# Performance work log

Measured on AMD Instinct MI355X. Metric: run time of the kernel, lower is better.

The kernel has to match this reference:

```python
import jax, jax.numpy as jnp
import numpy as np

# Reconstructed Int8Conv2d semantics (repo internals not shown):
#  - input quantized to int8 with running scale: q = clip(round(x/scale), -128, 127)
#  - int8 weights (integer-valued fp32 here), int32 accumulation via conv
#  - dequantize with scale*W_SCALE; propagated scale gains a fixed requant
#    factor RQ so next layer's int8 quantization stays in range.
W_SCALE = 0.05   # per-layer weight quantization scale
RQ = 16.0        # fixed requantization gain folded into propagated scale
INIT_SCALE = 0.05


def _round(x):
    return jnp.round(x)


def quant8(x, scale):
    return jnp.clip(_round(x / scale), -128.0, 127.0)


def conv2d(x, w, stride):
    # x: NHWC, w: HWIO, VALID padding
    return jax.lax.conv_general_dilated(
        x, w, window_strides=(stride, stride), padding='VALID',
        dimension_numbers=('NHWC', 'HWIO', 'NHWC'))


def int8_conv(scale, x, w8, stride=1):
    x8 = quant8(x, scale)                 # emulated int8
    acc = conv2d(x8, w8, stride)          # emulated int32 accumulate
    y = acc * (scale * W_SCALE)           # dequantize
    return scale * W_SCALE * RQ, y


def qmax_pool2d(x, k, s):
    return jax.lax.reduce_window(
        x, -jnp.inf, jax.lax.max,
        window_dimensions=(1, k, k, 1), window_strides=(1, s, s, 1),
        padding='VALID')


def setup_inputs() -> dict:
    key = jax.random.key(0)
    ks = jax.random.split(key, 5)
    B = 32768
    x = jax.random.uniform(ks[0], (B, 784), dtype=jnp.float32)
    # int8-valued weights stored as float32 (small range keeps int8 path unsaturated)
    w1 = jax.random.randint(ks[1], (3, 3, 4, 4), -8, 9).astype(jnp.float32)
    w2 = jax.random.randint(ks[2], (3, 3, 4, 4), -8, 9).astype(jnp.float32)
    w3 = jax.random.randint(ks[3], (3, 3, 4, 4), -8, 9).astype(jnp.float32)
    w4 = jax.random.randint(ks[4], (1, 1, 4, 12), -8, 9).astype(jnp.float32)
    return {'x': x, 'w1': w1, 'w2': w2, 'w3': w3, 'w4': w4}


def reference(x, w1, w2, w3, w4):
    B = x.shape[0]
    # reshape(-1,1,28,28,1) + pad last dim to 4  ==  NHWC with C=4 (3 zero channels)
    h = x.reshape(B, 28, 28, 1)
    h = jnp.pad(h, ((0, 0), (0, 0), (0, 0), (0, 3)))

    scale, h = int8_conv(INIT_SCALE, h, w1)      # -> 26x26x4
    h = qmax_pool2d(h, 2, 2)                      # -> 13x13
    h = jax.nn.relu(h)
    scale, h = int8_conv(scale, h, w2)            # -> 11x11
    h = qmax_pool2d(h, 2, 2)                      # -> 5x5
    h = jax.nn.relu(h)
    scale, h = int8_conv(scale, h, w3)            # -> 3x3
    h = qmax_pool2d(h, 3, 1)                      # -> 1x1
    h = jax.nn.relu(h)
    scale, h = int8_conv(scale, h, w4)            # -> 1x1x12
    h = jax.nn.relu(h)
    # (B,1,1,12) -> (B,12) -> drop last 2 -> (B,10)
    return h.reshape(B, 12)[:, :10]
```

## Files before the change

### kernel.cpp

```cpp
#include <hip/hip_runtime.h>
#include <hip/hip_bf16.h>

#define IPB 4

constexpr double dDQ1 = 0.05 * 0.05;
constexpr double dDQ2 = 0.05 * 0.05 * 16.0 * 0.05;
constexpr double dDQ3 = 0.05 * 0.05 * 16.0 * 0.05 * 16.0 * 0.05;
constexpr double dDQ4 = 0.05 * 0.05 * 16.0 * 0.05 * 16.0 * 0.05 * 16.0 * 0.05;

#define R1f 20.0f
#define R2f 25.0f
#define R3f 31.2499980926513671875f
#define R4f 39.0625f

#if __has_builtin(__builtin_amdgcn_sdot4)
__device__ __forceinline__ int dot4(int a, int b, int c) {
    return __builtin_amdgcn_sdot4(a, b, c, false);
}
#else
__device__ __forceinline__ int dot4(int a, int b, int c) {
    #pragma unroll
    for (int k = 0; k < 4; ++k)
        c += (int)(signed char)(a >> (8 * k)) * (int)(signed char)(b >> (8 * k));
    return c;
}
#endif

__device__ __forceinline__ void wave_fence() {
    __builtin_amdgcn_fence(__ATOMIC_ACQ_REL, "workgroup");
}

__device__ __forceinline__ float bfr(float f) {
    unsigned int u = __builtin_bit_cast(unsigned int, f);
    u += 0x7fffu + ((u >> 16) & 1u);
    u &= 0xffff0000u;
    return __builtin_bit_cast(float, u);
}

__device__ __forceinline__ int packq(float4 v) {
    int b0 = (int)rintf(v.x * R1f);
    int b1 = (int)rintf(v.y * R1f);
    int b2 = (int)rintf(v.z * R1f);
    int b3 = (int)rintf(v.w * R1f);
    return b0 | (b1 << 8) | (b2 << 16) | (b3 << 24);
}

__global__ void qcnn_prep(const float* __restrict__ w1, const float* __restrict__ w2,
                          const float* __restrict__ w3, const float* __restrict__ w4,
                          int* __restrict__ wpk) {
    int t = threadIdx.x;
    if (t < 24) {
        int oc = t / 6, rem = t % 6, r = rem >> 1, sh = rem & 1;
        int v = 0;
        #pragma unroll
        for (int k = 0; k < 4; ++k) {
            int kw = k - sh;
            int w = (kw >= 0 && kw < 3) ? (int)w1[(r * 3 + kw) * 16 + oc] : 0;
            v |= (w & 0xff) << (8 * k);
        }
        wpk[t] = v;
    } else if (t < 60) {
        int e = t - 24, tap = e >> 2, oc = e & 3, v = 0;
        #pragma unroll
        for (int k = 0; k < 4; ++k) v |= (((int)w2[tap * 16 + k * 4 + oc]) & 0xff) << (8 * k);
        wpk[t] = v;
    } else if (t < 96) {
        int e = t - 60, tap = e >> 2, oc = e & 3, v = 0;
        #pragma unroll
        for (int k = 0; k < 4; ++k) v |= (((int)w3[tap * 16 + k * 4 + oc]) & 0xff) << (8 * k);
        wpk[t] = v;
    } else if (t < 108) {
        int col = t - 96, v = 0;
        #pragma unroll
        for (int k = 0; k < 4; ++k) v |= (((int)w4[k * 12 + col]) & 0xff) << (8 * k);
        wpk[t] = v;
    }
}

__global__ __launch_bounds__(256, 8) void qcnn_main(
    const float* __restrict__ x,
    const int* __restrict__ wpk,
    float* __restrict__ out, int B)
{
    __shared__ int q1a[IPB][196];
    __shared__ int q1b[IPB][196];
    __shared__ int q2c[IPB][169];
    __shared__ int q3c[IPB][25];
    __shared__ int c3s[IPB][36];
    __shared__ int q4d[IPB];

    const int tid = threadIdx.x, slot = tid >> 6, lane = tid & 63;
    const int img = blockIdx.x * IPB + slot;
    const bool valid = img < B;
    const float DQ1 = (float)dDQ1, DQ2 = (float)dDQ2, DQ3 = (float)dDQ3, DQ4 = (float)dDQ4;

    if (valid) {
        const float4* x4 = (const float4*)(x + (size_t)img * 784);
        float4 v0 = x4[lane];
        float4 v1 = x4[lane + 64];
        float4 v2 = x4[lane + 128];
        float4 v3 = (lane < 4) ? x4[lane + 192] : make_float4(0.f, 0.f, 0.f, 0.f);
        q1a[slot][lane]       = packq(v0);
        q1a[slot][lane + 64]  = packq(v1);
        q1a[slot][lane + 128] = packq(v2);
        if (lane < 4) q1a[slot][lane + 192] = packq(v3);
    }
    wave_fence();

    if (valid) {
        #pragma unroll
        for (int i = 0; i < 3; ++i) {
            int n = lane + 64 * i;
            if (n < 168) {
                int row = n / 6, j = n - row * 6;
                unsigned a = (unsigned)q1a[slot][row * 7 + j];
                unsigned b = (unsigned)q1a[slot][row * 7 + j + 1];
                q1b[slot][row * 7 + j] = (int)((a >> 16) | (b << 16));
            }
        }
    }
    wave_fence();

    if (valid) {
        int W1[24];
        #pragma unroll
        for (int i = 0; i < 24; ++i) W1[i] = wpk[i];
        #pragma unroll
        for (int it = 0; it < 3; ++it) {
            int cell = lane + 64 * it;
            if (cell < 169) {
                int ph = cell / 13, pw = cell - ph * 13;
                int r0 = 2 * ph, c0 = 2 * pw;
                const char* bp = (const char*)((c0 & 2) ? q1b[slot] : q1a[slot])
                                 + r0 * 28 + (c0 & ~3);
                int rw0 = *(const int*)(bp);
                int rw1 = *(const int*)(bp + 28);
                int rw2 = *(const int*)(bp + 56);
                int rw3 = *(const int*)(bp + 84);
                int outb = 0;
                #pragma unroll
                for (int oc = 0; oc < 4; ++oc) {
                    int a00 = 0, a01 = 0, a10 = 0, a11 = 0;
                    #pragma unroll
                    for (int r = 0; r < 3; ++r) {
                        int rwA = (r == 0) ? rw0 : ((r == 1) ? rw1 : rw2);
                        int rwB = (r == 0) ? rw1 : ((r == 1) ? rw2 : rw3);
                        a00 = dot4(rwA, W1[oc * 6 + r * 2 + 0], a00);
                        a01 = dot4(rwA, W1[oc * 6 + r * 2 + 1], a01);
                        a10 = dot4(rwB, W1[oc * 6 + r * 2 + 0], a10);
                        a11 = dot4(rwB, W1[oc * 6 + r * 2 + 1], a11);
                    }
                    int m = max(max(a00, a01), max(a10, a11));
                    float y = fmaxf((float)m * DQ1, 0.f);
                    outb |= ((int)rintf(y * R2f)) << (8 * oc);
                }
                q2c[slot][cell] = outb;
            }
        }
    }
    wave_fence();

    {
        int W2[36];
        #pragma unroll
        for (int i = 0; i < 36; ++i) W2[i] = wpk[24 + i];
        #pragma unroll
        for (int base_it = 0; base_it < 128; base_it += 64) {
            int it = base_it + lane;
            int a0 = 0, a1 = 0, a2 = 0, a3 = 0;
            int cell = 0, pos = 0;
            bool act = valid && it < 100;
            if (act) {
                cell = it >> 2; pos = it & 3;
                int ph = cell / 5, pw = cell - ph * 5;
                int ib = (2 * ph + (pos >> 1)) * 13 + 2 * pw + (pos & 1);
                const int* p = &q2c[slot][ib];
                #pragma unroll
                for (int kh = 0; kh < 3; ++kh)
                    #pragma unroll
                    for (int kw = 0; kw < 3; ++kw) {
                        int d = p[kh * 13 + kw];
                        a0 = dot4(d, W2[(kh * 3 + kw) * 4 + 0], a0);
                        a1 = dot4(d, W2[(kh * 3 + kw) * 4 + 1], a1);
                        a2 = dot4(d, W2[(kh * 3 + kw) * 4 + 2], a2);
                        a3 = dot4(d, W2[(kh * 3 + kw) * 4 + 3], a3);
                    }
            }
            int m0 = a0, m1 = a1, m2 = a2, m3 = a3;
            m0 = max(m0, __shfl_xor(m0, 1)); m0 = max(m0, __shfl_xor(m0, 2));
            m1 = max(m1, __shfl_xor(m1, 1)); m1 = max(m1, __shfl_xor(m1, 2));
            m2 = max(m2, __shfl_xor(m2, 1)); m2 = max(m2, __shfl_xor(m2, 2));
            m3 = max(m3, __shfl_xor(m3, 1)); m3 = max(m3, __shfl_xor(m3, 2));
            if (act && pos == 0) {
                int outb = 0;
                int mm[4] = {m0, m1, m2, m3};
                #pragma unroll
                for (int oc = 0; oc < 4; ++oc) {
                    float y = fmaxf((float)mm[oc] * DQ2, 0.f);
                    float t = fminf(rintf(y * R3f), 127.f);
                    outb |= ((int)t) << (8 * oc);
                }
                q3c[slot][cell] = outb;
            }
        }
    }
    wave_fence();

    if (valid && lane < 36) {
        int oc = lane & 3, pos = lane >> 2;
        int oh = pos / 3, ow = pos - oh * 3;
        const int* p = &q3c[slot][oh * 5 + ow];
        int a = 0;
        #pragma unroll
        for (int kh = 0; kh < 3; ++kh)
            #pragma unroll
            for (int kw = 0; kw < 3; ++kw)
                a = dot4(p[kh * 5 + kw], wpk[60 + (kh * 3 + kw) * 4 + oc], a);
        c3s[slot][lane] = a;
    }
    wave_fence();

    if (valid && lane < 4) {
        int m = c3s[slot][lane];
        #pragma unroll
        for (int p2 = 1; p2 < 9; ++p2) m = max(m, c3s[slot][p2 * 4 + lane]);
        float y = fmaxf((float)m * DQ3, 0.f);
        float t = fminf(rintf(y * R4f), 127.f);
        ((char*)&q4d[slot])[lane] = (char)(int)t;
    }
    wave_fence();

    if (valid && lane < 10) {
        int a = dot4(q4d[slot], wpk[96 + lane], 0);
        float y = fmaxf((float)a * DQ4, 0.f);
        out[(size_t)img * 10 + lane] = bfr(y);
    }
}

extern "C" void kernel_launch(void* const* d_in, const int* in_sizes, int n_in,
                              void* d_out, int out_size, void* d_ws, size_t ws_size,
                              hipStream_t stream) {
    (void)n_in; (void)ws_size; (void)out_size;
    const float* x  = (const float*)d_in[0];
    const float* w1 = (const float*)d_in[1];
    const float* w2 = (const float*)d_in[2];
    const float* w3 = (const float*)d_in[3];
    const float* w4 = (const float*)d_in[4];
    int* wpk = (int*)d_ws;
    float* out = (float*)d_out;

    const int B = in_sizes[0] / 784;
    qcnn_prep<<<1, 128, 0, stream>>>(w1, w2, w3, w4, wpk);
    qcnn_main<<<(B + IPB - 1) / IPB, 256, 0, stream>>>(x, wpk, out, B);
}
```

Baseline: 161.4 us.

## Drop shifted LDS copy, fuse conv3 pool via shuffles, use cvt_pk_u8 packing

```diff
diff --git a/kernel.cpp b/kernel.cpp
--- a/kernel.cpp
+++ b/kernel.cpp
@@ -26,6 +26,14 @@
 }
 #endif
 
+__device__ __forceinline__ unsigned pk_u8(float f, unsigned sel, unsigned old) {
+#if __has_builtin(__builtin_amdgcn_cvt_pk_u8_f32)
+    return __builtin_amdgcn_cvt_pk_u8_f32(f, sel, old);
+#else
+    return old | (((unsigned)(int)f & 0xffu) << (8u * sel));
+#endif
+}
+
 __device__ __forceinline__ void wave_fence() {
     __builtin_amdgcn_fence(__ATOMIC_ACQ_REL, "workgroup");
 }
@@ -38,11 +46,11 @@
 }
 
 __device__ __forceinline__ int packq(float4 v) {
-    int b0 = (int)rintf(v.x * R1f);
-    int b1 = (int)rintf(v.y * R1f);
-    int b2 = (int)rintf(v.z * R1f);
-    int b3 = (int)rintf(v.w * R1f);
-    return b0 | (b1 << 8) | (b2 << 16) | (b3 << 24);
+    unsigned r = pk_u8(rintf(v.x * R1f), 0u, 0u);
+    r = pk_u8(rintf(v.y * R1f), 1u, r);
+    r = pk_u8(rintf(v.z * R1f), 2u, r);
+    r = pk_u8(rintf(v.w * R1f), 3u, r);
+    return (int)r;
 }
 
 __global__ void qcnn_prep(const float* __restrict__ w1, const float* __restrict__ w2,
@@ -82,12 +90,9 @@
     const int* __restrict__ wpk,
     float* __restrict__ out, int B)
 {
-    __shared__ int q1a[IPB][196];
-    __shared__ int q1b[IPB][196];
+    __shared__ int q1a[IPB][200];
     __shared__ int q2c[IPB][169];
     __shared__ int q3c[IPB][25];
-    __shared__ int c3s[IPB][36];
-    __shared__ int q4d[IPB];
 
     const int tid = threadIdx.x, slot = tid >> 6, lane = tid & 63;
     const int img = blockIdx.x * IPB + slot;
@@ -108,20 +113,6 @@
     wave_fence();
 
     if (valid) {
-        #pragma unroll
-        for (int i = 0; i < 3; ++i) {
-            int n = lane + 64 * i;
-            if (n < 168) {
-                int row = n / 6, j = n - row * 6;
-                unsigned a = (unsigned)q1a[slot][row * 7 + j];
-                unsigned b = (unsigned)q1a[slot][row * 7 + j + 1];
-                q1b[slot][row * 7 + j] = (int)((a >> 16) | (b << 16));
-            }
-        }
-    }
-    wave_fence();
-
-    if (valid) {
         int W1[24];
         #pragma unroll
         for (int i = 0; i < 24; ++i) W1[i] = wpk[i];
@@ -131,30 +122,31 @@
             if (cell < 169) {
                 int ph = cell / 13, pw = cell - ph * 13;
                 int r0 = 2 * ph, c0 = 2 * pw;
-                const char* bp = (const char*)((c0 & 2) ? q1b[slot] : q1a[slot])
-                                 + r0 * 28 + (c0 & ~3);
-                int rw0 = *(const int*)(bp);
-                int rw1 = *(const int*)(bp + 28);
-                int rw2 = *(const int*)(bp + 56);
-                int rw3 = *(const int*)(bp + 84);
-                int outb = 0;
+                bool odd = (c0 & 2) != 0;
+                const int* bp = &q1a[slot][r0 * 7 + (c0 >> 2)];
+                int rw[4];
+                #pragma unroll
+                for (int r = 0; r < 4; ++r) {
+                    int a = bp[r * 7], b = bp[r * 7 + 1];
+                    int sh = (int)(((unsigned)a >> 16) | ((unsigned)b << 16));
+                    rw[r] = odd ? sh : a;
+                }
+                unsigned outb = 0;
                 #pragma unroll
                 for (int oc = 0; oc < 4; ++oc) {
                     int a00 = 0, a01 = 0, a10 = 0, a11 = 0;
                     #pragma unroll
                     for (int r = 0; r < 3; ++r) {
-                        int rwA = (r == 0) ? rw0 : ((r == 1) ? rw1 : rw2);
-                        int rwB = (r == 0) ? rw1 : ((r == 1) ? rw2 : rw3);
-                        a00 = dot4(rwA, W1[oc * 6 + r * 2 + 0], a00);
-                        a01 = dot4(rwA, W1[oc * 6 + r * 2 + 1], a01);
-                        a10 = dot4(rwB, W1[oc * 6 + r * 2 + 0], a10);
-                        a11 = dot4(rwB, W1[oc * 6 + r * 2 + 1], a11);
+                        a00 = dot4(rw[r],     W1[oc * 6 + r * 2 + 0], a00);
+                        a01 = dot4(rw[r],     W1[oc * 6 + r * 2 + 1], a01);
+                        a10 = dot4(rw[r + 1], W1[oc * 6 + r * 2 + 0], a10);
+                        a11 = dot4(rw[r + 1], W1[oc * 6 + r * 2 + 1], a11);
                     }
                     int m = max(max(a00, a01), max(a10, a11));
                     float y = fmaxf((float)m * DQ1, 0.f);
-                    outb |= ((int)rintf(y * R2f)) << (8 * oc);
+                    outb = pk_u8(rintf(y * R2f), (unsigned)oc, outb);
                 }
-                q2c[slot][cell] = outb;
+                q2c[slot][cell] = (int)outb;
             }
         }
     }
@@ -192,47 +184,42 @@
             m2 = max(m2, __shfl_xor(m2, 1)); m2 = max(m2, __shfl_xor(m2, 2));
             m3 = max(m3, __shfl_xor(m3, 1)); m3 = max(m3, __shfl_xor(m3, 2));
             if (act && pos == 0) {
-                int outb = 0;
+                unsigned outb = 0;
                 int mm[4] = {m0, m1, m2, m3};
                 #pragma unroll
                 for (int oc = 0; oc < 4; ++oc) {
                     float y = fmaxf((float)mm[oc] * DQ2, 0.f);
                     float t = fminf(rintf(y * R3f), 127.f);
-                    outb |= ((int)t) << (8 * oc);
+                    outb = pk_u8(t, (unsigned)oc, outb);
                 }
-                q3c[slot][cell] = outb;
+                q3c[slot][cell] = (int)outb;
             }
         }
     }
     wave_fence();
 
+    int a3 = (int)0x80000000u;
     if (valid && lane < 36) {
         int oc = lane & 3, pos = lane >> 2;
         int oh = pos / 3, ow = pos - oh * 3;
         const int* p = &q3c[slot][oh * 5 + ow];
-        int a = 0;
+        a3 = 0;
         #pragma unroll
         for (int kh = 0; kh < 3; ++kh)
             #pragma unroll
             for (int kw = 0; kw < 3; ++kw)
-                a = dot4(p[kh * 5 + kw], wpk[60 + (kh * 3 + kw) * 4 + oc], a);
-        c3s[slot][lane] = a;
-    }
-    wave_fence();
-
-    if (valid && lane < 4) {
-        int m = c3s[slot][lane];
-        #pragma unroll
-        for (int p2 = 1; p2 < 9; ++p2) m = max(m, c3s[slot][p2 * 4 + lane]);
-        float y = fmaxf((float)m * DQ3, 0.f);
-        float t = fminf(rintf(y * R4f), 127.f);
-        ((char*)&q4d[slot])[lane] = (char)(int)t;
-    }
-    wave_fence();
-
+                a3 = dot4(p[kh * 5 + kw], wpk[60 + (kh * 3 + kw) * 4 + oc], a3);
+    }
+    #pragma unroll
+    for (int s = 4; s <= 32; s <<= 1) a3 = max(a3, __shfl_xor(a3, s));
+    float y3 = fmaxf((float)a3 * DQ3, 0.f);
+    float t3 = fminf(rintf(y3 * R4f), 127.f);
+    int b4 = (int)pk_u8(t3, (unsigned)(lane & 3), 0u);
+    b4 |= __shfl_xor(b4, 1);
+    b4 |= __shfl_xor(b4, 2);
     if (valid && lane < 10) {
-        int a = dot4(q4d[slot], wpk[96 + lane], 0);
-        float y = fmaxf((float)a * DQ4, 0.f);
+        int a4 = dot4(b4, wpk[96 + lane], 0);
+        float y = fmaxf((float)a4 * DQ4, 0.f);
         out[(size_t)img * 10 + lane] = bfr(y);
     }
 }
```

After: 161.3 us. About the same (-0.1%).
